# Optimization experiments

Hardware: AMD Instinct MI355X
Metric: run time of the kernel (lower is better)

## Reference

```python
import jax, jax.numpy as jnp
import numpy as np

N_SEQ, N_RES, C_M = 512, 384, 256
C_O, C_Z = 32, 128  # num_outer_channel, num_output_channel
LN_EPS = 1e-5
NORM_EPS = 1e-3


def setup_inputs() -> dict:
    key = jax.random.key(0)
    ks = jax.random.split(key, 8)
    scale = 1.0 / np.sqrt(C_M)
    return {
        "act": jax.random.normal(ks[0], (N_SEQ, N_RES, C_M), dtype=jnp.float32),
        "mask": jax.random.uniform(ks[1], (N_SEQ, N_RES), dtype=jnp.float32),
        "ln_w": jnp.ones((C_M,), dtype=jnp.float32),
        "ln_b": jnp.zeros((C_M,), dtype=jnp.float32),
        "left_w": jax.random.normal(ks[2], (C_O, C_M), dtype=jnp.float32) * scale,
        "left_b": jnp.zeros((C_O,), dtype=jnp.float32),
        "right_w": jax.random.normal(ks[3], (C_O, C_M), dtype=jnp.float32) * scale,
        "right_b": jnp.zeros((C_O,), dtype=jnp.float32),
        "output_w": jax.random.normal(ks[4], (C_O, C_O, C_Z), dtype=jnp.float32) * (1.0 / C_O),
        "output_b": jnp.zeros((C_Z,), dtype=jnp.float32),
    }


def reference(act, mask, ln_w, ln_b, left_w, left_b, right_w, right_b, output_w, output_b):
    # LayerNorm over c_m
    mu = jnp.mean(act, axis=-1, keepdims=True)
    var = jnp.var(act, axis=-1, keepdims=True)
    act_n = (act - mu) * jax.lax.rsqrt(var + LN_EPS) * ln_w + ln_b

    m = mask[..., None]  # [s, r, 1]
    left = m * (jnp.einsum("src,oc->sro", act_n, left_w) + left_b)    # [s, r, co]
    right = m * (jnp.einsum("src,oc->sro", act_n, right_w) + right_b)  # [s, r, co]

    # outer product over sequence dim, then contract with output_w:
    # out[b, d, f] = sum_{a, c, e} left[a, b, c] * right[a, d, e] * w[c, e, f]
    outer = jnp.einsum("abc,ade->bdce", left, right)          # [r, r, co, co]
    out = jnp.einsum("bdce,cef->bdf", outer, output_w) + output_b  # [r, r, c_z]

    norm = jnp.einsum("sb,sd->bd", mask, mask)[..., None]  # [r, r, 1]
    return out / (NORM_EPS + norm)
```

## Files before the change

kernel.cpp:

```cpp
#include <hip/hip_runtime.h>

typedef short short8 __attribute__((ext_vector_type(8)));
typedef short short4v __attribute__((ext_vector_type(4)));
typedef float f32x4 __attribute__((ext_vector_type(4)));
typedef unsigned short ushort_t;

#define DEV_INLINE __device__ __forceinline__

constexpr int NSEQ = 512, NRES = 384, CM = 256, CO = 32, CZ = 128;
constexpr float F_LN_EPS = 1e-5f, F_NORM_EPS = 1e-3f;

constexpr size_t WS_LT   = 0;
constexpr size_t WS_RT   = WS_LT + (size_t)12288 * 512 * 2;
constexpr size_t WS_WT   = WS_RT + (size_t)12288 * 512 * 2;
constexpr size_t WS_NORM = WS_WT + (size_t)128 * 1024 * 2;
constexpr size_t WS_PW   = WS_NORM + (size_t)384 * 384 * 4;

DEV_INLINE ushort_t f2bf(float x) {
  union { float f; unsigned u; } v; v.f = x;
  unsigned r = v.u + 0x7FFFu + ((v.u >> 16) & 1u);
  return (ushort_t)(r >> 16);
}

DEV_INLINE short8 pack8(float4 a, float4 b) {
  short8 p;
  p[0] = (short)f2bf(a.x); p[1] = (short)f2bf(a.y);
  p[2] = (short)f2bf(a.z); p[3] = (short)f2bf(a.w);
  p[4] = (short)f2bf(b.x); p[5] = (short)f2bf(b.y);
  p[6] = (short)f2bf(b.z); p[7] = (short)f2bf(b.w);
  return p;
}

DEV_INLINE void async16(const void* g, void* l) {
  __builtin_amdgcn_global_load_lds(
      (const __attribute__((address_space(1))) unsigned*)g,
      (__attribute__((address_space(3))) unsigned*)l, 16, 0, 0);
}

__global__ __launch_bounds__(256) void k_wt(const float* __restrict__ W,
                                            ushort_t* __restrict__ WT) {
  int tid = blockIdx.x * 256 + threadIdx.x;
  int f = tid >> 10, ce = tid & 1023;
  WT[tid] = f2bf(W[(size_t)ce * CZ + f]);
}

__global__ __launch_bounds__(256) void k_pack(const float* __restrict__ left_w,
                                              const float* __restrict__ right_w,
                                              ushort_t* __restrict__ PW) {
  int id = blockIdx.x * 256 + threadIdx.x;
  int o = id >> 5, ch = id & 31;
  const float* src = (o < 32 ? left_w + (size_t)o * CM
                             : right_w + (size_t)(o - 32) * CM) + ch * 8;
  float4 a = *(const float4*)src, b = *(const float4*)(src + 4);
  *(short8*)&PW[(size_t)o * CM + ch * 8] = pack8(a, b);
}

__global__ __launch_bounds__(256) void k_norm(const float* __restrict__ mask,
                                              float* __restrict__ normM) {
  int b = blockIdx.x * 16 + threadIdx.x;
  int d = blockIdx.y * 16 + threadIdx.y;
  float a0 = 0.f, a1 = 0.f, a2 = 0.f, a3 = 0.f;
  for (int a = 0; a < NSEQ; a += 4) {
    a0 += mask[(size_t)(a + 0) * NRES + b] * mask[(size_t)(a + 0) * NRES + d];
    a1 += mask[(size_t)(a + 1) * NRES + b] * mask[(size_t)(a + 1) * NRES + d];
    a2 += mask[(size_t)(a + 2) * NRES + b] * mask[(size_t)(a + 2) * NRES + d];
    a3 += mask[(size_t)(a + 3) * NRES + b] * mask[(size_t)(a + 3) * NRES + d];
  }
  normM[(size_t)b * NRES + d] = (a0 + a1) + (a2 + a3);
}

__global__ __launch_bounds__(256) void k_lnproj(
    const float* __restrict__ act, const float* __restrict__ mask,
    const float* __restrict__ ln_w, const float* __restrict__ ln_b,
    const float* __restrict__ left_b, const float* __restrict__ right_b,
    const ushort_t* __restrict__ PW,
    ushort_t* __restrict__ Lt, ushort_t* __restrict__ Rt) {
  __shared__ ushort_t sAct[16 * 256];

  const int t = threadIdx.x;
  const int a0 = blockIdx.x * 16;
  const int b = blockIdx.y;
  const int r = t >> 4, c = t & 15;

  const float4* arow =
      (const float4*)(act + ((size_t)(a0 + r) * NRES + b) * CM + c * 16);
  float4 v[4];
  float s = 0.f, ss = 0.f;
#pragma unroll
  for (int j = 0; j < 4; j++) {
    v[j] = arow[j];
    s += v[j].x + v[j].y + v[j].z + v[j].w;
    ss += v[j].x * v[j].x + v[j].y * v[j].y + v[j].z * v[j].z + v[j].w * v[j].w;
  }
  s += __shfl_xor(s, 1);  s += __shfl_xor(s, 2);
  s += __shfl_xor(s, 4);  s += __shfl_xor(s, 8);
  ss += __shfl_xor(ss, 1); ss += __shfl_xor(ss, 2);
  ss += __shfl_xor(ss, 4); ss += __shfl_xor(ss, 8);
  const float mu = s * (1.f / CM);
  const float rs = rsqrtf(ss * (1.f / CM) - mu * mu + F_LN_EPS);

  const int lane = t & 63, w = t >> 6;
  const int q = lane >> 4, ln = lane & 15;
  short8 bfrag[8];
#pragma unroll
  for (int ks = 0; ks < 8; ks++)
    bfrag[ks] = *(const short8*)&PW[(size_t)(w * 16 + ln) * CM + (ks * 4 + q) * 8];

#pragma unroll
  for (int j = 0; j < 2; j++) {
    int cb = c * 16 + j * 8;
    float4 lw0 = *(const float4*)(ln_w + cb), lw1 = *(const float4*)(ln_w + cb + 4);
    float4 lb0 = *(const float4*)(ln_b + cb), lb1 = *(const float4*)(ln_b + cb + 4);
    float4 x0 = v[2 * j], x1 = v[2 * j + 1], y0, y1;
    y0.x = (x0.x - mu) * rs * lw0.x + lb0.x;
    y0.y = (x0.y - mu) * rs * lw0.y + lb0.y;
    y0.z = (x0.z - mu) * rs * lw0.z + lb0.z;
    y0.w = (x0.w - mu) * rs * lw0.w + lb0.w;
    y1.x = (x1.x - mu) * rs * lw1.x + lb1.x;
    y1.y = (x1.y - mu) * rs * lw1.y + lb1.y;
    y1.z = (x1.z - mu) * rs * lw1.z + lb1.z;
    y1.w = (x1.w - mu) * rs * lw1.w + lb1.w;
    int chunk = c * 2 + j;
    *(short8*)&sAct[r * 256 + ((chunk ^ (r & 7)) * 8)] = pack8(y0, y1);
  }
  __syncthreads();

  f32x4 acc = {0, 0, 0, 0};
#pragma unroll
  for (int ks = 0; ks < 8; ks++) {
    int kc = ks * 4 + q;
    short8 af = *(const short8*)&sAct[ln * 256 + ((kc ^ (ln & 7)) * 8)];
    acc = __builtin_amdgcn_mfma_f32_16x16x32_bf16(af, bfrag[ks], acc, 0, 0, 0);
  }

  const int o = w * 16 + ln;
  float mk[4];
#pragma unroll
  for (int reg = 0; reg < 4; reg++)
    mk[reg] = mask[(size_t)(a0 + q * 4 + reg) * NRES + b];
  float bias = (o < 32) ? left_b[o] : right_b[o - 32];
  ushort_t* dst = (o < 32) ? (Lt + (size_t)(b * 32 + o) * NSEQ)
                           : (Rt + (size_t)(b * 32 + (o - 32)) * NSEQ);
  short4v pk;
#pragma unroll
  for (int reg = 0; reg < 4; reg++)
    pk[reg] = (short)f2bf((acc[reg] + bias) * mk[reg]);
  *(short4v*)&dst[a0 + q * 4] = pk;
}

__global__ __launch_bounds__(256, 3) void k_opm(
    const ushort_t* __restrict__ Lt, const ushort_t* __restrict__ Rt,
    const ushort_t* __restrict__ WT, const float* __restrict__ normM,
    const float* __restrict__ out_b, float* __restrict__ out) {
  __shared__ ushort_t smem[24576];
  ushort_t* sA = smem;
  ushort_t* sB = smem + 8192;
  ushort_t* sP = smem;
  ushort_t* sW = smem + 16384;

  const int t = threadIdx.x, lane = t & 63, w = t >> 6;
  const int q = lane >> 4, ln = lane & 15;
  const int wm = w & 1, wn = w >> 1;
  const int m0 = blockIdx.x * 128, n0 = blockIdx.y * 128;
  const int srow8 = lane >> 3, schunk = lane & 7;

  f32x4 acc1[4][4];
#pragma unroll
  for (int i = 0; i < 4; i++)
#pragma unroll
    for (int j = 0; j < 4; j++) acc1[i][j] = {0, 0, 0, 0};

  for (int kt = 0; kt < 8; kt++) {
    __syncthreads();
#pragma unroll
    for (int i = 0; i < 4; i++) {
      int rg = w + i * 4;
      int r = rg * 8 + srow8;
      int gc = schunk ^ (r & 7);
      async16(Lt + (size_t)(m0 + r) * NSEQ + kt * 64 + gc * 8, (char*)sA + rg * 1024);
      async16(Rt + (size_t)(n0 + r) * NSEQ + kt * 64 + gc * 8, (char*)sB + rg * 1024);
    }
    __syncthreads();
#pragma unroll
    for (int ks = 0; ks < 2; ks++) {
      int kc = ks * 4 + q;
      short8 af[4], bf[4];
#pragma unroll
      for (int tm = 0; tm < 4; tm++) {
        int rr = wm * 64 + tm * 16 + ln;
        af[tm] = *(const short8*)&sA[rr * 64 + ((kc ^ (rr & 7)) * 8)];
      }
#pragma unroll
      for (int tn = 0; tn < 4; tn++) {
        int rr = wn * 64 + tn * 16 + ln;
        bf[tn] = *(const short8*)&sB[rr * 64 + ((kc ^ (rr & 7)) * 8)];
      }
#pragma unroll
      for (int tm = 0; tm < 4; tm++)
#pragma unroll
        for (int tn = 0; tn < 4; tn++)
          acc1[tm][tn] =
              __builtin_amdgcn_mfma_f32_16x16x32_bf16(af[tm], bf[tn], acc1[tm][tn], 0, 0, 0);
    }
  }

  __syncthreads();
#pragma unroll
  for (int tm = 0; tm < 4; tm++) {
#pragma unroll
    for (int tn = 0; tn < 4; tn++) {
      int pair = (wm * 2 + (tm >> 1)) * 4 + (wn * 2 + (tn >> 1));
      int e = (tn & 1) * 16 + ln;
#pragma unroll
      for (int reg = 0; reg < 4; reg++) {
        int c = (tm & 1) * 16 + q * 4 + reg;
        int ce = c * 32 + e;
        int pos = (ce >> 3) ^ (pair & 7);
        sP[pair * 1024 + pos * 8 + (ce & 7)] = f2bf(acc1[tm][tn][reg]);
      }
    }
  }
  __syncthreads();

  f32x4 acc2[2] = {{0, 0, 0, 0}, {0, 0, 0, 0}};
  for (int kt = 0; kt < 16; kt++) {
    if (kt) __syncthreads();
#pragma unroll
    for (int i = 0; i < 4; i++) {
      int rg = w + i * 4;
      int r = rg * 8 + srow8;
      int gc = schunk ^ (r & 7);
      async16(WT + (size_t)r * 1024 + kt * 64 + gc * 8, (char*)sW + rg * 1024);
    }
    __syncthreads();
#pragma unroll
    for (int ks = 0; ks < 2; ks++) {
      int pchunk = kt * 8 + ks * 4 + q;
      short8 af = *(const short8*)&sP[ln * 1024 + ((pchunk ^ (ln & 7)) * 8)];
      int kc = ks * 4 + q;
#pragma unroll
      for (int tn = 0; tn < 2; tn++) {
        int fr = w * 32 + tn * 16 + ln;
        short8 bf = *(const short8*)&sW[fr * 64 + ((kc ^ (fr & 7)) * 8)];
        acc2[tn] = __builtin_amdgcn_mfma_f32_16x16x32_bf16(af, bf, acc2[tn], 0, 0, 0);
      }
    }
  }

  const int b = blockIdx.x * 4 + q;
#pragma unroll
  for (int reg = 0; reg < 4; reg++) {
    int d = blockIdx.y * 4 + reg;
    float inv = 1.f / (F_NORM_EPS + normM[(size_t)b * NRES + d]);
#pragma unroll
    for (int tn = 0; tn < 2; tn++) {
      int f = w * 32 + tn * 16 + ln;
      out[((size_t)b * NRES + d) * CZ + f] = (acc2[tn][reg] + out_b[f]) * inv;
    }
  }
}

extern "C" void kernel_launch(void* const* d_in, const int* in_sizes, int n_in,
                              void* d_out, int out_size, void* d_ws, size_t ws_size,
                              hipStream_t stream) {
  (void)in_sizes; (void)n_in; (void)out_size; (void)ws_size;
  const float* act      = (const float*)d_in[0];
  const float* mask     = (const float*)d_in[1];
  const float* ln_w     = (const float*)d_in[2];
  const float* ln_b     = (const float*)d_in[3];
  const float* left_w   = (const float*)d_in[4];
  const float* left_b   = (const float*)d_in[5];
  const float* right_w  = (const float*)d_in[6];
  const float* right_b  = (const float*)d_in[7];
  const float* output_w = (const float*)d_in[8];
  const float* output_b = (const float*)d_in[9];
  float* out = (float*)d_out;

  char* ws = (char*)d_ws;
  ushort_t* Lt = (ushort_t*)(ws + WS_LT);
  ushort_t* Rt = (ushort_t*)(ws + WS_RT);
  ushort_t* WT = (ushort_t*)(ws + WS_WT);
  float* normM = (float*)(ws + WS_NORM);
  ushort_t* PW = (ushort_t*)(ws + WS_PW);

  hipLaunchKernelGGL(k_pack, dim3(8), dim3(256), 0, stream, left_w, right_w, PW);
  hipLaunchKernelGGL(k_wt, dim3(512), dim3(256), 0, stream, output_w, WT);
  hipLaunchKernelGGL(k_norm, dim3(24, 24), dim3(16, 16), 0, stream, mask, normM);
  hipLaunchKernelGGL(k_lnproj, dim3(32, 384), dim3(256), 0, stream, act, mask,
                     ln_w, ln_b, left_b, right_b, PW, Lt, Rt);
  hipLaunchKernelGGL(k_opm, dim3(96, 96), dim3(256), 0, stream, Lt, Rt, WT,
                     normM, output_b, out);
}
```

Before: 607.8 us.

## Read output weights directly from global memory and coalesce LayerNorm act loads

The second GEMM stage in k_opm now loads output-weight fragments straight from global memory (through cache) into registers instead of staging them through shared memory with two barriers per k-step. This cuts shared memory from 48KB to 32KB, and launch bounds are raised to allow 4 blocks per SM. Separately, k_lnproj reorders its act loads so neighbouring threads read contiguous float4s, and writes bf16 in 4-element pieces. Uncoalesced global weight reads and more register pressure are the risks.

Result: slower. 756.5 us (+24.5%).

```diff
diff --git a/kernel.cpp b/kernel.cpp
--- a/kernel.cpp
+++ b/kernel.cpp
@@ -82,13 +82,12 @@
   const int b = blockIdx.y;
   const int r = t >> 4, c = t & 15;
 
-  const float4* arow =
-      (const float4*)(act + ((size_t)(a0 + r) * NRES + b) * CM + c * 16);
+  const float* rowp = act + ((size_t)(a0 + r) * NRES + b) * CM;
   float4 v[4];
   float s = 0.f, ss = 0.f;
 #pragma unroll
   for (int j = 0; j < 4; j++) {
-    v[j] = arow[j];
+    v[j] = *(const float4*)(rowp + j * 64 + c * 4);
     s += v[j].x + v[j].y + v[j].z + v[j].w;
     ss += v[j].x * v[j].x + v[j].y * v[j].y + v[j].z * v[j].z + v[j].w * v[j].w;
   }
@@ -107,21 +106,18 @@
     bfrag[ks] = *(const short8*)&PW[(size_t)(w * 16 + ln) * CM + (ks * 4 + q) * 8];
 
 #pragma unroll
-  for (int j = 0; j < 2; j++) {
-    int cb = c * 16 + j * 8;
-    float4 lw0 = *(const float4*)(ln_w + cb), lw1 = *(const float4*)(ln_w + cb + 4);
-    float4 lb0 = *(const float4*)(ln_b + cb), lb1 = *(const float4*)(ln_b + cb + 4);
-    float4 x0 = v[2 * j], x1 = v[2 * j + 1], y0, y1;
-    y0.x = (x0.x - mu) * rs * lw0.x + lb0.x;
-    y0.y = (x0.y - mu) * rs * lw0.y + lb0.y;
-    y0.z = (x0.z - mu) * rs * lw0.z + lb0.z;
-    y0.w = (x0.w - mu) * rs * lw0.w + lb0.w;
-    y1.x = (x1.x - mu) * rs * lw1.x + lb1.x;
-    y1.y = (x1.y - mu) * rs * lw1.y + lb1.y;
-    y1.z = (x1.z - mu) * rs * lw1.z + lb1.z;
-    y1.w = (x1.w - mu) * rs * lw1.w + lb1.w;
-    int chunk = c * 2 + j;
-    *(short8*)&sAct[r * 256 + ((chunk ^ (r & 7)) * 8)] = pack8(y0, y1);
+  for (int j = 0; j < 4; j++) {
+    int cb = j * 64 + c * 4;
+    float4 lw = *(const float4*)(ln_w + cb);
+    float4 lb = *(const float4*)(ln_b + cb);
+    float4 x = v[j];
+    short4v p;
+    p[0] = (short)f2bf((x.x - mu) * rs * lw.x + lb.x);
+    p[1] = (short)f2bf((x.y - mu) * rs * lw.y + lb.y);
+    p[2] = (short)f2bf((x.z - mu) * rs * lw.z + lb.z);
+    p[3] = (short)f2bf((x.w - mu) * rs * lw.w + lb.w);
+    int chunk = j * 8 + (c >> 1);
+    *(short4v*)&sAct[r * 256 + ((chunk ^ (r & 7)) * 8) + (c & 1) * 4] = p;
   }
   __syncthreads();
 
@@ -148,15 +144,14 @@
   *(short4v*)&dst[a0 + q * 4] = pk;
 }
 
-__global__ __launch_bounds__(256, 3) void k_opm(
+__global__ __launch_bounds__(256, 4) void k_opm(
     const ushort_t* __restrict__ Lt, const ushort_t* __restrict__ Rt,
     const ushort_t* __restrict__ WT, const float* __restrict__ normM,
     const float* __restrict__ out_b, float* __restrict__ out) {
-  __shared__ ushort_t smem[24576];
+  __shared__ ushort_t smem[16384];
   ushort_t* sA = smem;
   ushort_t* sB = smem + 8192;
   ushort_t* sP = smem;
-  ushort_t* sW = smem + 16384;
 
   const int t = threadIdx.x, lane = t & 63, w = t >> 6;
   const int q = lane >> 4, ln = lane & 15;
@@ -223,27 +218,18 @@
   __syncthreads();
 
   f32x4 acc2[2] = {{0, 0, 0, 0}, {0, 0, 0, 0}};
+  const ushort_t* wb0 = WT + (size_t)(w * 32 + ln) * 1024 + q * 8;
+  const ushort_t* wb1 = wb0 + (size_t)16 * 1024;
+#pragma unroll
   for (int kt = 0; kt < 16; kt++) {
-    if (kt) __syncthreads();
-#pragma unroll
-    for (int i = 0; i < 4; i++) {
-      int rg = w + i * 4;
-      int r = rg * 8 + srow8;
-      int gc = schunk ^ (r & 7);
-      async16(WT + (size_t)r * 1024 + kt * 64 + gc * 8, (char*)sW + rg * 1024);
-    }
-    __syncthreads();
 #pragma unroll
     for (int ks = 0; ks < 2; ks++) {
       int pchunk = kt * 8 + ks * 4 + q;
       short8 af = *(const short8*)&sP[ln * 1024 + ((pchunk ^ (ln & 7)) * 8)];
-      int kc = ks * 4 + q;
-#pragma unroll
-      for (int tn = 0; tn < 2; tn++) {
-        int fr = w * 32 + tn * 16 + ln;
-        short8 bf = *(const short8*)&sW[fr * 64 + ((kc ^ (fr & 7)) * 8)];
-        acc2[tn] = __builtin_amdgcn_mfma_f32_16x16x32_bf16(af, bf, acc2[tn], 0, 0, 0);
-      }
+      short8 b0 = *(const short8*)(wb0 + kt * 64 + ks * 32);
+      short8 b1 = *(const short8*)(wb1 + kt * 64 + ks * 32);
+      acc2[0] = __builtin_amdgcn_mfma_f32_16x16x32_bf16(af, b0, acc2[0], 0, 0, 0);
+      acc2[1] = __builtin_amdgcn_mfma_f32_16x16x32_bf16(af, b1, acc2[1], 0, 0, 0);
     }
   }
 
```
